# Optimization experiments

Hardware: AMD Instinct MI355X
Metric: run time of the kernel (lower is better)

## Reference

```python
import math
import jax, jax.numpy as jnp
import numpy as np

DIM = 2048
N_HEADS = 16
HEAD_DIM = DIM // N_HEADS  # 128
BSZ = 2
SEQLEN = 2048
ROPE_THETA = 500000.0


def _make_freqs(seqlen, head_dim, theta):
    inv = 1.0 / (theta ** (np.arange(0, head_dim, 2, dtype=np.float32) / head_dim))
    t = np.arange(seqlen, dtype=np.float32)
    f = np.outer(t, inv)  # [S, hd//2]
    return jnp.asarray(np.cos(f)), jnp.asarray(np.sin(f))


def setup_inputs() -> dict:
    key = jax.random.key(0)
    kx, kq, kk, kv, ko = jax.random.split(key, 5)
    scale = 0.02
    x = jax.random.normal(kx, (BSZ, SEQLEN, DIM), dtype=jnp.float32)
    wq = jax.random.normal(kq, (DIM, DIM), dtype=jnp.float32) * scale
    wk = jax.random.normal(kk, (DIM, DIM), dtype=jnp.float32) * scale
    wv = jax.random.normal(kv, (DIM, DIM), dtype=jnp.float32) * scale
    wo = jax.random.normal(ko, (DIM, DIM), dtype=jnp.float32) * scale
    freqs_cos, freqs_sin = _make_freqs(SEQLEN, HEAD_DIM, ROPE_THETA)
    # causal additive mask: 0 on/below diag, -inf above
    mask = jnp.triu(jnp.full((SEQLEN, SEQLEN), float('-inf'), dtype=jnp.float32), k=1)
    return {"x": x, "start_pos": 0, "freqs_cos": freqs_cos, "freqs_sin": freqs_sin,
            "mask": mask, "wq": wq, "wk": wk, "wv": wv, "wo": wo}


def _apply_rope(t, cos, sin):
    # t: [B, S, H, hd]; cos/sin: [S, hd//2]
    b, s, h, hd = t.shape
    tr = t.reshape(b, s, h, hd // 2, 2)
    a, bb = tr[..., 0], tr[..., 1]
    c = cos[None, :, None, :]
    sn = sin[None, :, None, :]
    out_r = a * c - bb * sn
    out_i = a * sn + bb * c
    return jnp.stack([out_r, out_i], axis=-1).reshape(b, s, h, hd)


def reference(x, start_pos, freqs_cos, freqs_sin, mask, wq, wk, wv, wo):
    b, s, _ = x.shape
    xq = (x @ wq.T).reshape(b, s, N_HEADS, HEAD_DIM)
    xk = (x @ wk.T).reshape(b, s, N_HEADS, HEAD_DIM)
    xv = (x @ wv.T).reshape(b, s, N_HEADS, HEAD_DIM)
    xq = _apply_rope(xq, freqs_cos, freqs_sin)
    xk = _apply_rope(xk, freqs_cos, freqs_sin)
    # [B, H, S, hd]
    xq = xq.transpose(0, 2, 1, 3)
    xk = xk.transpose(0, 2, 1, 3)
    xv = xv.transpose(0, 2, 1, 3)
    scores = jnp.einsum('bhqd,bhkd->bhqk', xq, xk) / math.sqrt(HEAD_DIM)
    scores = scores + mask[None, None, :, :]
    probs = jax.nn.softmax(scores.astype(jnp.float32), axis=-1).astype(xq.dtype)
    out = jnp.einsum('bhqk,bhkd->bhqd', probs, xv)
    out = out.transpose(0, 2, 1, 3).reshape(b, s, -1)
    return out @ wo.T
```

## Files before the change

### kernel.cpp

```cpp
#include <hip/hip_runtime.h>
#include <stdint.h>

#define DIM 2048
#define SEQ 2048
#define NHEADS 16
#define HDIM 128
#define BSZ 2
#define ROWS (BSZ*SEQ)

typedef uint16_t u16;
typedef __attribute__((ext_vector_type(8))) short bf16x8;
typedef __attribute__((ext_vector_type(4))) short bf16x4;
typedef __attribute__((ext_vector_type(4))) float fx4;
typedef __attribute__((ext_vector_type(4))) uint16_t u16x4;

typedef const __attribute__((address_space(1))) uint32_t* gp_t;
typedef __attribute__((address_space(3))) uint32_t* lp_t;
#define GLL16(g, l) __builtin_amdgcn_global_load_lds((gp_t)(g), (lp_t)(l), 16, 0, 0)

__device__ inline u16 f2bf(float f) {
  union { float f; uint32_t u; } v; v.f = f;
  uint32_t u = v.u;
  u += 0x7FFFu + ((u >> 16) & 1u);
  return (u16)(u >> 16);
}
__device__ inline float bf2f(u16 h) {
  union { uint32_t u; float f; } v; v.u = ((uint32_t)h) << 16;
  return v.f;
}

__global__ __launch_bounds__(256) void cvt5_kernel(const float* __restrict__ sx,
    const float* __restrict__ s1, const float* __restrict__ s2,
    const float* __restrict__ s3, const float* __restrict__ s4,
    u16* __restrict__ dst) {
  const int XC = (ROWS * DIM) / 4;
  const int WC = (DIM * DIM) / 4;
  int i = blockIdx.x * 256 + threadIdx.x;
  const float* src;
  int off;
  if (i < XC) { src = sx; off = i; }
  else {
    int t = i - XC;
    int w = t >> 20;
    off = t & (WC - 1);
    src = (w == 0) ? s1 : (w == 1) ? s2 : (w == 2) ? s3 : s4;
  }
  fx4 f = *(const fx4*)(src + (size_t)off * 4);
  u16x4 o;
  o[0] = f2bf(f[0]); o[1] = f2bf(f[1]); o[2] = f2bf(f[2]); o[3] = f2bf(f[3]);
  *(u16x4*)(dst + (size_t)i * 4) = o;
}

#define BM 256
#define BN 128
#define BK 64
#define NT (DIM / BK)
#define BUFSZ ((BM + BN) * BK)

__global__ __launch_bounds__(512, 2) void gemm_qkv8(const u16* __restrict__ A,
    const u16* __restrict__ B0, const u16* __restrict__ B1, const u16* __restrict__ B2,
    u16* __restrict__ C0, u16* __restrict__ C1, u16* __restrict__ vtg,
    const float* __restrict__ fcos, const float* __restrict__ fsin) {
  __shared__ __align__(16) u16 sm[2 * BUFSZ];

  const int tid  = threadIdx.x;
  const int lane = tid & 63, wave = tid >> 6;
  const int l16  = lane & 15, quad = lane >> 4;
  const int wm   = wave >> 2;
  const int wn   = wave & 3;

  int t = (blockIdx.x & 7) * 96 + (blockIdx.x >> 3);
  const int z   = t >> 8;
  const int rem = t & 255;
  const int M0  = (rem >> 4) * BM;
  const int N0  = (rem & 15) * BN;
  const u16* B = (z == 0) ? B0 : (z == 1) ? B1 : B2;

  const int u0 = tid, u1 = 512 + tid;
  const int rl0 = u0 >> 3, ch0 = (u0 & 7) ^ (rl0 & 7);
  const int rl1 = u1 >> 3, ch1 = (u1 & 7) ^ (rl1 & 7);

  const int sw  = l16 & 7;
  const int ka0 = (quad ^ sw) * 8;
  const int ka1 = ((4 + quad) ^ sw) * 8;
  const int rowA = (wm * 128 + l16) * BK;
  const int rowB = (wn * 32  + l16) * BK;

#define STGA(h, kt2) do { if ((kt2) < NT) {                                              \
    const u16* _g = A + (size_t)(M0 + (h) * 128) * DIM + (kt2) * BK;                     \
    u16* _l = sm + ((kt2) & 1) * BUFSZ + (h) * 8192 + wave * 512;                        \
    GLL16(_g + (size_t)rl0 * DIM + ch0 * 8, _l);                                         \
    GLL16(_g + (size_t)rl1 * DIM + ch1 * 8, _l + 4096); } } while (0)
#define STGB(kt2) do { if ((kt2) < NT) {                                                 \
    const u16* _g = B + (size_t)N0 * DIM + (kt2) * BK;                                   \
    u16* _l = sm + ((kt2) & 1) * BUFSZ + 16384 + wave * 512;                             \
    GLL16(_g + (size_t)rl0 * DIM + ch0 * 8, _l);                                         \
    GLL16(_g + (size_t)rl1 * DIM + ch1 * 8, _l + 4096); } } while (0)

  STGB(0); STGA(0, 0); STGA(1, 0);
  STGB(1); STGA(0, 1);
  asm volatile("s_waitcnt vmcnt(4)" ::: "memory");
  __builtin_amdgcn_s_barrier();

  fx4 acc[8][2];
#pragma unroll
  for (int m = 0; m < 8; ++m)
#pragma unroll
    for (int n = 0; n < 2; ++n) acc[m][n] = fx4{0.f, 0.f, 0.f, 0.f};

  bf16x8 af[4][2], b0[2], b1[2];

  for (int kt = 0; kt < NT; ++kt) {
    const u16* Ab = sm + (kt & 1) * BUFSZ;
    const u16* Bb = Ab + 16384;

#pragma unroll
    for (int m = 0; m < 4; ++m) {
      af[m][0] = *(const bf16x8*)(Ab + rowA + m * (16 * BK) + ka0);
      af[m][1] = *(const bf16x8*)(Ab + rowA + m * (16 * BK) + ka1);
    }
    b0[0] = *(const bf16x8*)(Bb + rowB + ka0);
    b0[1] = *(const bf16x8*)(Bb + rowB + ka1);
    STGA(1, kt + 1);
    asm volatile("s_waitcnt lgkmcnt(8)" ::: "memory");
    __builtin_amdgcn_sched_barrier(0);
    __builtin_amdgcn_s_barrier();
    asm volatile("s_waitcnt lgkmcnt(0)" ::: "memory");
    __builtin_amdgcn_sched_barrier(0);
    __builtin_amdgcn_s_setprio(1);
#pragma unroll
    for (int m = 0; m < 4; ++m) {
      acc[m][0] = __builtin_amdgcn_mfma_f32_16x16x32_bf16(af[m][0], b0[0], acc[m][0], 0, 0, 0);
      acc[m][0] = __builtin_amdgcn_mfma_f32_16x16x32_bf16(af[m][1], b0[1], acc[m][0], 0, 0, 0);
    }
    __builtin_amdgcn_s_setprio(0);
    __builtin_amdgcn_s_barrier();

    b1[0] = *(const bf16x8*)(Bb + rowB + 16 * BK + ka0);
    b1[1] = *(const bf16x8*)(Bb + rowB + 16 * BK + ka1);
    __builtin_amdgcn_s_barrier();
    asm volatile("s_waitcnt lgkmcnt(0)" ::: "memory");
    __builtin_amdgcn_sched_barrier(0);
    __builtin_amdgcn_s_setprio(1);
#pragma unroll
    for (int m = 0; m < 4; ++m) {
      acc[m][1] = __builtin_amdgcn_mfma_f32_16x16x32_bf16(af[m][0], b1[0], acc[m][1], 0, 0, 0);
      acc[m][1] = __builtin_amdgcn_mfma_f32_16x16x32_bf16(af[m][1], b1[1], acc[m][1], 0, 0, 0);
    }
    __builtin_amdgcn_s_setprio(0);
    __builtin_amdgcn_s_barrier();

#pragma unroll
    for (int m = 0; m < 4; ++m) {
      af[m][0] = *(const bf16x8*)(Ab + rowA + (m + 4) * (16 * BK) + ka0);
      af[m][1] = *(const bf16x8*)(Ab + rowA + (m + 4) * (16 * BK) + ka1);
    }
    STGB(kt + 2);
    __builtin_amdgcn_s_barrier();
    asm volatile("s_waitcnt lgkmcnt(0)" ::: "memory");
    __builtin_amdgcn_sched_barrier(0);
    __builtin_amdgcn_s_setprio(1);
#pragma unroll
    for (int m = 0; m < 4; ++m) {
      acc[m + 4][1] = __builtin_amdgcn_mfma_f32_16x16x32_bf16(af[m][0], b1[0], acc[m + 4][1], 0, 0, 0);
      acc[m + 4][1] = __builtin_amdgcn_mfma_f32_16x16x32_bf16(af[m][1], b1[1], acc[m + 4][1], 0, 0, 0);
    }
    __builtin_amdgcn_s_setprio(0);
    __builtin_amdgcn_s_barrier();

    STGA(0, kt + 2);
    __builtin_amdgcn_s_barrier();
    __builtin_amdgcn_s_setprio(1);
#pragma unroll
    for (int m = 0; m < 4; ++m) {
      acc[m + 4][0] = __builtin_amdgcn_mfma_f32_16x16x32_bf16(af[m][0], b0[0], acc[m + 4][0], 0, 0, 0);
      acc[m + 4][0] = __builtin_amdgcn_mfma_f32_16x16x32_bf16(af[m][1], b0[1], acc[m + 4][0], 0, 0, 0);
    }
    __builtin_amdgcn_s_setprio(0);
    if (kt < NT - 2) asm volatile("s_waitcnt vmcnt(4)" ::: "memory");
    else             asm volatile("s_waitcnt vmcnt(0)" ::: "memory");
    __builtin_amdgcn_sched_barrier(0);
    __builtin_amdgcn_s_barrier();
  }
#undef STGA
#undef STGB

  if (z < 2) {
    u16* C = (z == 0) ? C0 : C1;
    u16* Cr = C + (size_t)(M0 + wm * 128 + quad * 4) * DIM + N0 + wn * 32 + l16;
#pragma unroll
    for (int mt = 0; mt < 8; ++mt)
#pragma unroll
      for (int r = 0; r < 4; ++r) {
        int s = (M0 + wm * 128 + mt * 16 + quad * 4 + r) & (SEQ - 1);
        const float* cb = fcos + s * 64;
        const float* sb = fsin + s * 64;
#pragma unroll
        for (int nt = 0; nt < 2; ++nt) {
          int p = (wn * 32 + nt * 16 + l16) >> 1;
          float val = acc[mt][nt][r];
          float par = __shfl_xor(val, 1);
          float c = cb[p], sn = sb[p];
          float out = (l16 & 1) ? (par * sn + val * c) : (val * c - par * sn);
          Cr[(size_t)(mt * 16 + r) * DIM + nt * 16] = f2bf(out);
        }
      }
  } else {
    u16 (*T)[256] = reinterpret_cast<u16 (*)[256]>(sm);
    __syncthreads();
#pragma unroll
    for (int mt = 0; mt < 8; ++mt)
#pragma unroll
      for (int nt = 0; nt < 2; ++nt) {
        int col = wn * 32 + nt * 16 + l16;
        int rowb = (wm * 128 + mt * 16 + quad * 4) ^ ((col & 7) << 3);
        u16x4 p;
        p[0] = f2bf(acc[mt][nt][0]); p[1] = f2bf(acc[mt][nt][1]);
        p[2] = f2bf(acc[mt][nt][2]); p[3] = f2bf(acc[mt][nt][3]);
        *(u16x4*)&T[col][rowb] = p;
      }
    __syncthreads();
    const int b  = M0 >> 11;
    const int s0 = M0 & (SEQ - 1);
    const int h  = N0 >> 7;
#pragma unroll
    for (int i = 0; i < 8; ++i) {
      int c = i * 512 + tid;
      int col = c >> 5;
      int s8 = (c & 31) * 8;
      bf16x8 v8 = *(const bf16x8*)&T[col][s8 ^ ((col & 7) << 3)];
      *(bf16x8*)(vtg + ((size_t)(b * NHEADS + h) * HDIM + col) * SEQ + s0 + s8) = v8;
    }
  }
}

__global__ __launch_bounds__(512, 2) void gemm_out8(const u16* __restrict__ A,
                                                    const u16* __restrict__ B,
                                                    float* __restrict__ C) {
  __shared__ __align__(16) u16 sm[2 * BUFSZ];

  const int tid  = threadIdx.x;
  const int lane = tid & 63, wave = tid >> 6;
  const int l16  = lane & 15, quad = lane >> 4;
  const int wm   = wave >> 2;
  const int wn   = wave & 3;

  int t = (blockIdx.x & 7) * 32 + (blockIdx.x >> 3);
  const int M0  = (t >> 4) * BM;
  const int N0  = (t & 15) * BN;

  const int u0 = tid, u1 = 512 + tid;
  const int rl0 = u0 >> 3, ch0 = (u0 & 7) ^ (rl0 & 7);
  const int rl1 = u1 >> 3, ch1 = (u1 & 7) ^ (rl1 & 7);

  const int sw  = l16 & 7;
  const int ka0 = (quad ^ sw) * 8;
  const int ka1 = ((4 + quad) ^ sw) * 8;
  const int rowA = (wm * 128 + l16) * BK;
  const int rowB = (wn * 32  + l16) * BK;

#define STGA(h, kt2) do { if ((kt2) < NT) {                                              \
    const u16* _g = A + (size_t)(M0 + (h) * 128) * DIM + (kt2) * BK;                     \
    u16* _l = sm + ((kt2) & 1) * BUFSZ + (h) * 8192 + wave * 512;                        \
    GLL16(_g + (size_t)rl0 * DIM + ch0 * 8, _l);                                         \
    GLL16(_g + (size_t)rl1 * DIM + ch1 * 8, _l + 4096); } } while (0)
#define STGB(kt2) do { if ((kt2) < NT) {                                                 \
    const u16* _g = B + (size_t)N0 * DIM + (kt2) * BK;                                   \
    u16* _l = sm + ((kt2) & 1) * BUFSZ + 16384 + wave * 512;                             \
    GLL16(_g + (size_t)rl0 * DIM + ch0 * 8, _l);                                         \
    GLL16(_g + (size_t)rl1 * DIM + ch1 * 8, _l + 4096); } } while (0)

  STGB(0); STGA(0, 0); STGA(1, 0);
  STGB(1); STGA(0, 1);
  asm volatile("s_waitcnt vmcnt(4)" ::: "memory");
  __builtin_amdgcn_s_barrier();

  fx4 acc[8][2];
#pragma unroll
  for (int m = 0; m < 8; ++m)
#pragma unroll
    for (int n = 0; n < 2; ++n) acc[m][n] = fx4{0.f, 0.f, 0.f, 0.f};

  bf16x8 af[4][2], b0[2], b1[2];

  for (int kt = 0; kt < NT; ++kt) {
    const u16* Ab = sm + (kt & 1) * BUFSZ;
    const u16* Bb = Ab + 16384;

#pragma unroll
    for (int m = 0; m < 4; ++m) {
      af[m][0] = *(const bf16x8*)(Ab + rowA + m * (16 * BK) + ka0);
      af[m][1] = *(const bf16x8*)(Ab + rowA + m * (16 * BK) + ka1);
    }
    b0[0] = *(const bf16x8*)(Bb + rowB + ka0);
    b0[1] = *(const bf16x8*)(Bb + rowB + ka1);
    STGA(1, kt + 1);
    asm volatile("s_waitcnt lgkmcnt(8)" ::: "memory");
    __builtin_amdgcn_sched_barrier(0);
    __builtin_amdgcn_s_barrier();
    asm volatile("s_waitcnt lgkmcnt(0)" ::: "memory");
    __builtin_amdgcn_sched_barrier(0);
    __builtin_amdgcn_s_setprio(1);
#pragma unroll
    for (int m = 0; m < 4; ++m) {
      acc[m][0] = __builtin_amdgcn_mfma_f32_16x16x32_bf16(af[m][0], b0[0], acc[m][0], 0, 0, 0);
      acc[m][0] = __builtin_amdgcn_mfma_f32_16x16x32_bf16(af[m][1], b0[1], acc[m][0], 0, 0, 0);
    }
    __builtin_amdgcn_s_setprio(0);
    __builtin_amdgcn_s_barrier();

    b1[0] = *(const bf16x8*)(Bb + rowB + 16 * BK + ka0);
    b1[1] = *(const bf16x8*)(Bb + rowB + 16 * BK + ka1);
    __builtin_amdgcn_s_barrier();
    asm volatile("s_waitcnt lgkmcnt(0)" ::: "memory");
    __builtin_amdgcn_sched_barrier(0);
    __builtin_amdgcn_s_setprio(1);
#pragma unroll
    for (int m = 0; m < 4; ++m) {
      acc[m][1] = __builtin_amdgcn_mfma_f32_16x16x32_bf16(af[m][0], b1[0], acc[m][1], 0, 0, 0);
      acc[m][1] = __builtin_amdgcn_mfma_f32_16x16x32_bf16(af[m][1], b1[1], acc[m][1], 0, 0, 0);
    }
    __builtin_amdgcn_s_setprio(0);
    __builtin_amdgcn_s_barrier();

#pragma unroll
    for (int m = 0; m < 4; ++m) {
      af[m][0] = *(const bf16x8*)(Ab + rowA + (m + 4) * (16 * BK) + ka0);
      af[m][1] = *(const bf16x8*)(Ab + rowA + (m + 4) * (16 * BK) + ka1);
    }
    STGB(kt + 2);
    __builtin_amdgcn_s_barrier();
    asm volatile("s_waitcnt lgkmcnt(0)" ::: "memory");
    __builtin_amdgcn_sched_barrier(0);
    __builtin_amdgcn_s_setprio(1);
#pragma unroll
    for (int m = 0; m < 4; ++m) {
      acc[m + 4][1] = __builtin_amdgcn_mfma_f32_16x16x32_bf16(af[m][0], b1[0], acc[m + 4][1], 0, 0, 0);
      acc[m + 4][1] = __builtin_amdgcn_mfma_f32_16x16x32_bf16(af[m][1], b1[1], acc[m + 4][1], 0, 0, 0);
    }
    __builtin_amdgcn_s_setprio(0);
    __builtin_amdgcn_s_barrier();

    STGA(0, kt + 2);
    __builtin_amdgcn_s_barrier();
    __builtin_amdgcn_s_setprio(1);
#pragma unroll
    for (int m = 0; m < 4; ++m) {
      acc[m + 4][0] = __builtin_amdgcn_mfma_f32_16x16x32_bf16(af[m][0], b0[0], acc[m + 4][0], 0, 0, 0);
      acc[m + 4][0] = __builtin_amdgcn_mfma_f32_16x16x32_bf16(af[m][1], b0[1], acc[m + 4][0], 0, 0, 0);
    }
    __builtin_amdgcn_s_setprio(0);
    if (kt < NT - 2) asm volatile("s_waitcnt vmcnt(4)" ::: "memory");
    else             asm volatile("s_waitcnt vmcnt(0)" ::: "memory");
    __builtin_amdgcn_sched_barrier(0);
    __builtin_amdgcn_s_barrier();
  }
#undef STGA
#undef STGB

  float* Cr = C + (size_t)(M0 + wm * 128 + quad * 4) * DIM + N0 + wn * 32 + l16;
#pragma unroll
  for (int mt = 0; mt < 8; ++mt)
#pragma unroll
    for (int nt = 0; nt < 2; ++nt)
#pragma unroll
      for (int r = 0; r < 4; ++r)
        Cr[(size_t)(mt * 16 + r) * DIM + nt * 16] = acc[mt][nt][r];
}

struct SMemS { u16 Ks[64][136]; u16 Vt[128][72]; };
union SMemU { SMemS s; u16 Ot[4][32][136]; };

__global__ __launch_bounds__(256, 2) void attn_kernel(const u16* __restrict__ qm,
                                                      const u16* __restrict__ km,
                                                      const u16* __restrict__ vtg,
                                                      u16* __restrict__ ao) {
  __shared__ __align__(16) SMemU sm;
  const int tid = threadIdx.x;
  const int lane = tid & 63, wave = tid >> 6;
  const int l16 = lane & 15, quad = lane >> 4;
  const int idx = blockIdx.x;
  const int bh = idx & 31;
  const int j = idx >> 5;
  const int qt = (j < 8) ? (15 - j) : (j - 8);
  const int b = bh >> 4, h = bh & 15;
  const int q0 = qt * 128;
  const size_t brow = (size_t)b * SEQ;
  const int hc = h * HDIM;
  const size_t vbase = (size_t)bh * HDIM * SEQ;
  const int nkt = 2 * qt + 2;

  bf16x8 aq[2][4];
#pragma unroll
  for (int nt = 0; nt < 2; ++nt) {
    size_t qbase = (brow + q0 + wave * 32 + nt * 16 + l16) * DIM + hc;
#pragma unroll
    for (int dc = 0; dc < 4; ++dc)
      aq[nt][dc] = *(const bf16x8*)(qm + qbase + dc * 32 + quad * 8);
  }
  fx4 o[2][8];
#pragma unroll
  for (int nt = 0; nt < 2; ++nt)
#pragma unroll
    for (int dt = 0; dt < 8; ++dt) o[nt][dt] = fx4{0.f, 0.f, 0.f, 0.f};
  float mr[2] = {-3e38f, -3e38f}, lr[2] = {0.f, 0.f};

  bf16x8 kreg[4], vreg[4];
#pragma unroll
  for (int i = 0; i < 4; ++i) {
    int c = i * 256 + tid;
    kreg[i] = *(const bf16x8*)(km + (brow + (c >> 4)) * DIM + hc + (c & 15) * 8);
    vreg[i] = *(const bf16x8*)(vtg + vbase + (size_t)(c >> 3) * SEQ + (c & 7) * 8);
  }

  for (int kt = 0; kt < nkt; ++kt) {
    __syncthreads();
#pragma unroll
    for (int i = 0; i < 4; ++i) {
      int c = i * 256 + tid;
      *(bf16x8*)&sm.s.Ks[c >> 4][(c & 15) * 8] = kreg[i];
      *(bf16x8*)&sm.s.Vt[c >> 3][(c & 7) * 8] = vreg[i];
    }
    __syncthreads();
    if (kt + 1 < nkt) {
      const int kv1 = (kt + 1) * 64;
#pragma unroll
      for (int i = 0; i < 4; ++i) {
        int c = i * 256 + tid;
        kreg[i] = *(const bf16x8*)(km + (brow + kv1 + (c >> 4)) * DIM + hc + (c & 15) * 8);
        vreg[i] = *(const bf16x8*)(vtg + vbase + (size_t)(c >> 3) * SEQ + kv1 + (c & 7) * 8);
      }
    }
    fx4 s[2][4];
#pragma unroll
    for (int tm = 0; tm < 4; ++tm) {
      fx4 a0 = fx4{0.f, 0.f, 0.f, 0.f}, a1 = fx4{0.f, 0.f, 0.f, 0.f};
#pragma unroll
      for (int dc = 0; dc < 4; ++dc) {
        bf16x8 kf = *(const bf16x8*)&sm.s.Ks[tm * 16 + l16][dc * 32 + quad * 8];
        a0 = __builtin_amdgcn_mfma_f32_16x16x32_bf16(kf, aq[0][dc], a0, 0, 0, 0);
        a1 = __builtin_amdgcn_mfma_f32_16x16x32_bf16(kf, aq[1][dc], a1, 0, 0, 0);
      }
      s[0][tm] = a0 * 0.08838834764831845f;
      s[1][tm] = a1 * 0.08838834764831845f;
    }
    if (kt >= nkt - 2) {
      const int kv0 = kt * 64;
#pragma unroll
      for (int nt = 0; nt < 2; ++nt) {
        int qpos = q0 + wave * 32 + nt * 16 + l16;
#pragma unroll
        for (int tm = 0; tm < 4; ++tm)
#pragma unroll
          for (int r = 0; r < 4; ++r)
            if (kv0 + tm * 16 + quad * 4 + r > qpos) s[nt][tm][r] = -1e30f;
      }
    }
    float alpha[2];
    bf16x4 pf[2][4];
#pragma unroll
    for (int nt = 0; nt < 2; ++nt) {
      float t = -3e38f;
#pragma unroll
      for (int tm = 0; tm < 4; ++tm)
        t = fmaxf(t, fmaxf(fmaxf(s[nt][tm][0], s[nt][tm][1]),
                           fmaxf(s[nt][tm][2], s[nt][tm][3])));
      t = fmaxf(t, __shfl_xor(t, 16));
      t = fmaxf(t, __shfl_xor(t, 32));
      float mnew = fmaxf(mr[nt], t);
      alpha[nt] = __expf(mr[nt] - mnew);
      float sum = 0.f;
#pragma unroll
      for (int tm = 0; tm < 4; ++tm) {
        fx4 p;
#pragma unroll
        for (int r = 0; r < 4; ++r) {
          p[r] = __expf(s[nt][tm][r] - mnew);
          sum += p[r];
        }
        bf16x4 pb;
        pb[0] = (short)f2bf(p[0]); pb[1] = (short)f2bf(p[1]);
        pb[2] = (short)f2bf(p[2]); pb[3] = (short)f2bf(p[3]);
        pf[nt][tm] = pb;
      }
      sum += __shfl_xor(sum, 16);
      sum += __shfl_xor(sum, 32);
      lr[nt] = lr[nt] * alpha[nt] + sum;
      mr[nt] = mnew;
#pragma unroll
      for (int dt = 0; dt < 8; ++dt) o[nt][dt] *= alpha[nt];
    }
#pragma unroll
    for (int tm = 0; tm < 4; ++tm) {
#pragma unroll
      for (int dt = 0; dt < 8; ++dt) {
        bf16x4 vf = *(const bf16x4*)&sm.s.Vt[dt * 16 + l16][tm * 16 + quad * 4];
        o[0][dt] = __builtin_amdgcn_mfma_f32_16x16x16bf16_1k(vf, pf[0][tm], o[0][dt], 0, 0, 0);
        o[1][dt] = __builtin_amdgcn_mfma_f32_16x16x16bf16_1k(vf, pf[1][tm], o[1][dt], 0, 0, 0);
      }
    }
  }
  __syncthreads();
#pragma unroll
  for (int nt = 0; nt < 2; ++nt) {
    float inv = 1.f / lr[nt];
#pragma unroll
    for (int dt = 0; dt < 8; ++dt) {
      fx4 v = o[nt][dt];
      u16x4 p;
      p[0] = f2bf(v[0] * inv); p[1] = f2bf(v[1] * inv);
      p[2] = f2bf(v[2] * inv); p[3] = f2bf(v[3] * inv);
      *(u16x4*)&sm.Ot[wave][nt * 16 + l16][dt * 16 + quad * 4] = p;
    }
  }
#pragma unroll
  for (int i = 0; i < 8; ++i) {
    int c = i * 64 + lane;
    int row = c >> 4;
    int ch = c & 15;
    bf16x8 t = *(const bf16x8*)&sm.Ot[wave][row][ch * 8];
    *(bf16x8*)(ao + (brow + q0 + wave * 32 + row) * DIM + hc + ch * 8) = t;
  }
}

extern "C" void kernel_launch(void* const* d_in, const int* in_sizes, int n_in,
                              void* d_out, int out_size, void* d_ws, size_t ws_size,
                              hipStream_t stream) {
  const float* x    = (const float*)d_in[0];
  const float* fcos = (const float*)d_in[2];
  const float* fsin = (const float*)d_in[3];
  const float* wq   = (const float*)d_in[5];
  const float* wk   = (const float*)d_in[6];
  const float* wv   = (const float*)d_in[7];
  const float* wo   = (const float*)d_in[8];
  float* out = (float*)d_out;

  const size_t XN = (size_t)ROWS * DIM;
  const size_t WN = (size_t)DIM * DIM;
  u16* ws  = (u16*)d_ws;
  u16* xb  = ws;
  u16* wqb = xb + XN;
  u16* wkb = wqb + WN;
  u16* wvb = wkb + WN;
  u16* wob = wvb + WN;
  u16* q   = wob + WN;
  u16* k   = q + XN;
  u16* vtg = k + XN;
  u16* ao  = vtg + XN;

  const int total_chunks = (int)((XN + 4 * WN) / 4);
  cvt5_kernel<<<total_chunks / 256, 256, 0, stream>>>(x, wq, wk, wv, wo, ws);

  gemm_qkv8<<<dim3(768), 512, 0, stream>>>(xb, wqb, wkb, wvb, q, k, vtg, fcos, fsin);

  attn_kernel<<<dim3(512), 256, 0, stream>>>(q, k, vtg, ao);

  gemm_out8<<<dim3(256), 512, 0, stream>>>(ao, wob, out);
}
```

Before: 388.4 us.

## Double-buffer K/V tiles in LDS and skip softmax rescale unless max grows

Turns the attention kernel's K/V shared-memory staging into a double buffer. The next tile is written to the alternate buffer while the current one is consumed, so each iteration needs one barrier instead of two. It also adds a lazy online-softmax rescale: the running max and accumulator scaling are updated only when some lane's new tile max exceeds the stored max by more than 8, which removes most exp and multiply work on the output accumulator. The cost is doubled LDS use per block, which may limit the two-blocks-per-CU occupancy target, plus a wave-wide vote; probabilities can reach up to e^8 before normalisation.

```diff
diff --git a/kernel.cpp b/kernel.cpp
--- a/kernel.cpp
+++ b/kernel.cpp
@@ -368,7 +368,7 @@
         Cr[(size_t)(mt * 16 + r) * DIM + nt * 16] = acc[mt][nt][r];
 }
 
-struct SMemS { u16 Ks[64][136]; u16 Vt[128][72]; };
+struct SMemS { u16 Ks[2][64][136]; u16 Vt[2][128][72]; };
 union SMemU { SMemS s; u16 Ot[4][32][136]; };
 
 __global__ __launch_bounds__(256, 2) void attn_kernel(const u16* __restrict__ qm,
@@ -412,23 +412,39 @@
     kreg[i] = *(const bf16x8*)(km + (brow + (c >> 4)) * DIM + hc + (c & 15) * 8);
     vreg[i] = *(const bf16x8*)(vtg + vbase + (size_t)(c >> 3) * SEQ + (c & 7) * 8);
   }
-
-  for (int kt = 0; kt < nkt; ++kt) {
-    __syncthreads();
+#pragma unroll
+  for (int i = 0; i < 4; ++i) {
+    int c = i * 256 + tid;
+    *(bf16x8*)&sm.s.Ks[0][c >> 4][(c & 15) * 8] = kreg[i];
+    *(bf16x8*)&sm.s.Vt[0][c >> 3][(c & 7) * 8] = vreg[i];
+  }
+  if (1 < nkt) {
 #pragma unroll
     for (int i = 0; i < 4; ++i) {
       int c = i * 256 + tid;
-      *(bf16x8*)&sm.s.Ks[c >> 4][(c & 15) * 8] = kreg[i];
-      *(bf16x8*)&sm.s.Vt[c >> 3][(c & 7) * 8] = vreg[i];
-    }
-    __syncthreads();
+      kreg[i] = *(const bf16x8*)(km + (brow + 64 + (c >> 4)) * DIM + hc + (c & 15) * 8);
+      vreg[i] = *(const bf16x8*)(vtg + vbase + (size_t)(c >> 3) * SEQ + 64 + (c & 7) * 8);
+    }
+  }
+  __syncthreads();
+
+  for (int kt = 0; kt < nkt; ++kt) {
+    const int cur = kt & 1;
     if (kt + 1 < nkt) {
-      const int kv1 = (kt + 1) * 64;
 #pragma unroll
       for (int i = 0; i < 4; ++i) {
         int c = i * 256 + tid;
-        kreg[i] = *(const bf16x8*)(km + (brow + kv1 + (c >> 4)) * DIM + hc + (c & 15) * 8);
-        vreg[i] = *(const bf16x8*)(vtg + vbase + (size_t)(c >> 3) * SEQ + kv1 + (c & 7) * 8);
+        *(bf16x8*)&sm.s.Ks[cur ^ 1][c >> 4][(c & 15) * 8] = kreg[i];
+        *(bf16x8*)&sm.s.Vt[cur ^ 1][c >> 3][(c & 7) * 8] = vreg[i];
+      }
+    }
+    if (kt + 2 < nkt) {
+      const int kv2 = (kt + 2) * 64;
+#pragma unroll
+      for (int i = 0; i < 4; ++i) {
+        int c = i * 256 + tid;
+        kreg[i] = *(const bf16x8*)(km + (brow + kv2 + (c >> 4)) * DIM + hc + (c & 15) * 8);
+        vreg[i] = *(const bf16x8*)(vtg + vbase + (size_t)(c >> 3) * SEQ + kv2 + (c & 7) * 8);
       }
     }
     fx4 s[2][4];
@@ -437,7 +453,7 @@
       fx4 a0 = fx4{0.f, 0.f, 0.f, 0.f}, a1 = fx4{0.f, 0.f, 0.f, 0.f};
 #pragma unroll
       for (int dc = 0; dc < 4; ++dc) {
-        bf16x8 kf = *(const bf16x8*)&sm.s.Ks[tm * 16 + l16][dc * 32 + quad * 8];
+        bf16x8 kf = *(const bf16x8*)&sm.s.Ks[cur][tm * 16 + l16][dc * 32 + quad * 8];
         a0 = __builtin_amdgcn_mfma_f32_16x16x32_bf16(kf, aq[0][dc], a0, 0, 0, 0);
         a1 = __builtin_amdgcn_mfma_f32_16x16x32_bf16(kf, aq[1][dc], a1, 0, 0, 0);
       }
@@ -456,7 +472,6 @@
             if (kv0 + tm * 16 + quad * 4 + r > qpos) s[nt][tm][r] = -1e30f;
       }
     }
-    float alpha[2];
     bf16x4 pf[2][4];
 #pragma unroll
     for (int nt = 0; nt < 2; ++nt) {
@@ -467,15 +482,21 @@
                            fmaxf(s[nt][tm][2], s[nt][tm][3])));
       t = fmaxf(t, __shfl_xor(t, 16));
       t = fmaxf(t, __shfl_xor(t, 32));
-      float mnew = fmaxf(mr[nt], t);
-      alpha[nt] = __expf(mr[nt] - mnew);
+      if (!__all(t - mr[nt] <= 8.f)) {
+        float mnew = fmaxf(mr[nt], t);
+        float alpha = __expf(mr[nt] - mnew);
+        lr[nt] *= alpha;
+        mr[nt] = mnew;
+#pragma unroll
+        for (int dt = 0; dt < 8; ++dt) o[nt][dt] *= alpha;
+      }
       float sum = 0.f;
 #pragma unroll
       for (int tm = 0; tm < 4; ++tm) {
         fx4 p;
 #pragma unroll
         for (int r = 0; r < 4; ++r) {
-          p[r] = __expf(s[nt][tm][r] - mnew);
+          p[r] = __expf(s[nt][tm][r] - mr[nt]);
           sum += p[r];
         }
         bf16x4 pb;
@@ -485,22 +506,19 @@
       }
       sum += __shfl_xor(sum, 16);
       sum += __shfl_xor(sum, 32);
-      lr[nt] = lr[nt] * alpha[nt] + sum;
-      mr[nt] = mnew;
-#pragma unroll
-      for (int dt = 0; dt < 8; ++dt) o[nt][dt] *= alpha[nt];
+      lr[nt] += sum;
     }
 #pragma unroll
     for (int tm = 0; tm < 4; ++tm) {
 #pragma unroll
       for (int dt = 0; dt < 8; ++dt) {
-        bf16x4 vf = *(const bf16x4*)&sm.s.Vt[dt * 16 + l16][tm * 16 + quad * 4];
+        bf16x4 vf = *(const bf16x4*)&sm.s.Vt[cur][dt * 16 + l16][tm * 16 + quad * 4];
         o[0][dt] = __builtin_amdgcn_mfma_f32_16x16x16bf16_1k(vf, pf[0][tm], o[0][dt], 0, 0, 0);
         o[1][dt] = __builtin_amdgcn_mfma_f32_16x16x16bf16_1k(vf, pf[1][tm], o[1][dt], 0, 0, 0);
       }
     }
-  }
-  __syncthreads();
+    __syncthreads();
+  }
 #pragma unroll
   for (int nt = 0; nt < 2; ++nt) {
     float inv = 1.f / lr[nt];
```

Result: no change. 387.5 us (-0.2%).
